# Kernel optimization log

Hardware: AMD Instinct MI355X
Metric: run time of the kernel (lower is better)

## Reference

```python
import jax, jax.numpy as jnp
import numpy as np

B, T, K, H, KS = 8, 2048, 64, 8, 5
PAD = KS - 1  # causal left padding (kernel_size - stride, stride=1)


def setup_inputs() -> dict:
    key = jax.random.key(0)
    ks = jax.random.split(key, 6)
    s = 0.02
    return {
        "x": jax.random.normal(ks[0], (B, T, K), jnp.float32),
        "wq": jax.random.normal(ks[1], (K * H, K, KS), jnp.float32) * s,
        "bq": jnp.zeros((K * H,), jnp.float32),
        "wk": jax.random.normal(ks[2], (K * H, K, KS), jnp.float32) * s,
        "bk": jnp.zeros((K * H,), jnp.float32),
        "wv": jax.random.normal(ks[3], (K * H, K, KS), jnp.float32) * s,
        "wu": jax.random.normal(ks[4], (K, K * H), jnp.float32) * s,
        "bu": jnp.zeros((K,), jnp.float32),
    }


def _causal_conv(x_bkt, w, b=None):
    # x_bkt: [b, k, t]; w: [out_ch, in_ch, ks]; left-pad for causality
    y = jax.lax.conv_general_dilated(
        x_bkt, w, window_strides=(1,), padding=[(PAD, 0)],
        dimension_numbers=("NCH", "OIH", "NCH"))
    if b is not None:
        y = y + b[None, :, None]
    return y


def reference(x, wq, bq, wk, bk, wv, wu, bu):
    b, t, k = x.shape
    xc = jnp.transpose(x, (0, 2, 1))  # [b, k, t]
    # conv output channels k*h are viewed as (k, h): head index varies fastest
    q = _causal_conv(xc, wq, bq).reshape(b, k, H, t)
    kk = _causal_conv(xc, wk, bk).reshape(b, k, H, t)
    v = _causal_conv(xc, wv).reshape(b, k, H, t)
    scale = k ** 0.25
    # scores: [b, h, t_q, t_k]
    w = jnp.einsum("bdht,bdhs->bhts", q / scale, kk / scale)
    mask = jnp.triu(jnp.ones((t, t), bool), 1)  # mask_next=True, mask_diag=False
    w = jnp.where(mask[None, None], -jnp.inf, w)
    w = jax.nn.softmax(w, axis=-1)
    out = jnp.einsum("bhts,bdhs->bthd", w, v)  # [b, t, h, k]
    out = out.reshape(b, t, H * k)  # concat order (h outer, k inner)
    return out @ wu.T + bu
```

## Files before the change

kernel.cpp:

```cpp
#include <hip/hip_runtime.h>
#include <hip/hip_bf16.h>

typedef __attribute__((ext_vector_type(8))) short bf16x8;
typedef __attribute__((ext_vector_type(4))) float f32x4;
typedef __attribute__((ext_vector_type(16))) float f32x16;
typedef __attribute__((ext_vector_type(4))) unsigned int u32x4;
typedef __attribute__((ext_vector_type(2))) unsigned int u32x2;

#define Bn 8
#define Tn 2048
#define Kn 64
#define Hn 8
#define KSn 5
#define CHn 512
#define TPADn 2052

__device__ __forceinline__ unsigned short f2bf(float f) {
    unsigned int x = __builtin_bit_cast(unsigned int, f);
    unsigned int r = (x + 0x7fffu + ((x >> 16) & 1u)) >> 16;
    return (unsigned short)r;
}

__device__ __forceinline__ unsigned int cvt_pk_bf16(float lo, float hi) {
    unsigned int r;
    asm("v_cvt_pk_bf16_f32 %0, %1, %2" : "=v"(r) : "v"(lo), "v"(hi));
    return r;
}

__device__ __forceinline__ float fast_exp2(float x) {
#if __has_builtin(__builtin_amdgcn_exp2f)
    return __builtin_amdgcn_exp2f(x);
#else
    float r;
    asm("v_exp_f32 %0, %1" : "=v"(r) : "v"(x));
    return r;
#endif
}

__device__ __forceinline__ float xhalf_max(float v) {
    return fmaxf(v, __shfl_xor(v, 32));
}
__device__ __forceinline__ float xhalf_add(float v) {
    return v + __shfl_xor(v, 32);
}

__device__ __forceinline__ u32x2 pl32swap(unsigned int x, unsigned int y) {
#if __has_builtin(__builtin_amdgcn_permlane32_swap)
    return __builtin_amdgcn_permlane32_swap(x, y, false, false);
#else
    unsigned int xs = (unsigned int)__shfl_xor((int)x, 32);
    unsigned int ys = (unsigned int)__shfl_xor((int)y, 32);
    int hi = (threadIdx.x & 63) >> 5;
    u32x2 r;
    r[0] = hi ? ys : x;
    r[1] = hi ? y : xs;
    return r;
#endif
}

__device__ __forceinline__ void gload_lds16(const void* g, void* l) {
    __builtin_amdgcn_global_load_lds(
        (const __attribute__((address_space(1))) void*)g,
        (__attribute__((address_space(3))) void*)l, 16, 0, 0);
}

__global__ void prep_kernel(const float* __restrict__ x,
                            const float* __restrict__ wq, const float* __restrict__ bq,
                            const float* __restrict__ wk, const float* __restrict__ bk,
                            const float* __restrict__ wv,
                            const float* __restrict__ wu,
                            unsigned short* __restrict__ x_pad,
                            unsigned short* __restrict__ w2q, unsigned short* __restrict__ w2k,
                            unsigned short* __restrict__ w2v,
                            unsigned short* __restrict__ wu_b,
                            float* __restrict__ bqs, float* __restrict__ bks)
{
    const float inv_scale = 0.424660900144f;
    const int N0 = Bn*TPADn*Kn;
    const int N1 = KSn*CHn*Kn;
    const int total = N0 + 3*N1 + CHn*Kn + 2*CHn;
    for (int i = blockIdx.x*blockDim.x + threadIdx.x; i < total; i += gridDim.x*blockDim.x) {
        if (i < N0) {
            int b = i / (TPADn*Kn);
            int rem = i - b*(TPADn*Kn);
            int p = rem >> 6, ic = rem & 63;
            x_pad[i] = (p < 4) ? (unsigned short)0
                               : f2bf(x[((size_t)b*Tn + (p - 4))*Kn + ic]);
            continue;
        }
        int r = i - N0;
        if (r < 3*N1) {
            int conv = r / N1; int rr = r - conv*N1;
            int j = rr / (CHn*Kn); int rc = rr - j*(CHn*Kn);
            int c = rc >> 6; int ic = rc & 63;
            const float* w = (conv==0) ? wq : ((conv==1) ? wk : wv);
            float s = (conv==2) ? 1.0f : inv_scale;
            unsigned short* dst = (conv==0) ? w2q : ((conv==1) ? w2k : w2v);
            dst[rr] = f2bf(w[(c*Kn + ic)*KSn + j] * s);
            continue;
        }
        r -= 3*N1;
        if (r < CHn*Kn) { wu_b[r] = f2bf(wu[r]); continue; }
        r -= CHn*Kn;
        if (r < CHn) { bqs[r] = bq[r]*inv_scale; continue; }
        r -= CHn;
        bks[r] = bk[r]*inv_scale;
    }
}

__global__ __launch_bounds__(256) void conv_v4(
    const unsigned short* __restrict__ x_pad,
    const unsigned short* __restrict__ w2q, const unsigned short* __restrict__ w2k,
    const unsigned short* __restrict__ w2v,
    const float* __restrict__ bqs, const float* __restrict__ bks,
    unsigned short* __restrict__ q_s, unsigned short* __restrict__ k_s,
    unsigned short* __restrict__ v_t)
{
    __shared__ __align__(16) unsigned short xs[2][72*64];
    __shared__ __align__(16) unsigned short ts[64*64];
    const int tg = blockIdx.x;
    const int c0 = blockIdx.y * 64;
    const int zz = blockIdx.z;
    const int conv = zz >> 3, b = zz & 7;
    const unsigned short* w2 = (conv==0) ? w2q : ((conv==1) ? w2k : w2v);
    const float* bias = (conv==0) ? bqs : ((conv==1) ? bks : nullptr);
    unsigned short* outp = (conv==0) ? q_s : ((conv==1) ? k_s : v_t);
    const int tid = threadIdx.x;
    const int wid = tid >> 6, l = tid & 63;
    const int lr = l & 15, lh = l >> 4;
    const int wt = wid & 1, wc = wid >> 1;

    bf16x8 wf[5][2][2];
    #pragma unroll
    for (int j = 0; j < 5; ++j)
        #pragma unroll
        for (int kk = 0; kk < 2; ++kk)
            #pragma unroll
            for (int n2 = 0; n2 < 2; ++n2)
                wf[j][kk][n2] = *(const bf16x8*)
                    &w2[(j*CHn + c0 + wc*32 + n2*16 + lr)*Kn + kk*32 + lh*8];
    float bv0 = bias ? bias[c0 + wc*32 + lr]      : 0.0f;
    float bv1 = bias ? bias[c0 + wc*32 + 16 + lr] : 0.0f;

    const int swz_row = l >> 3;
    const int src_inrow = ((l & 7) << 4) ^ (swz_row << 4);

    int buf = 0;
    {
        const char* base = (const char*)(x_pad + (size_t)b*TPADn*Kn);
        int p0 = tg*512;
        for (int i = wid; i < 9; i += 4) {
            const char* src = base + (size_t)(p0 + i*8 + swz_row)*128 + src_inrow;
            gload_lds16(src, (char*)&xs[0][0] + i*1024);
        }
    }
    __syncthreads();

    for (int tt = 0; tt < 8; ++tt) {
        const int t0 = (tg*8 + tt)*64;
        if (tt < 7) {
            const char* base = (const char*)(x_pad + (size_t)b*TPADn*Kn);
            int p0 = t0 + 64;
            for (int i = wid; i < 9; i += 4) {
                const char* src = base + (size_t)(p0 + i*8 + swz_row)*128 + src_inrow;
                gload_lds16(src, (char*)&xs[buf^1][0] + i*1024);
            }
        }
        const char* xb = (const char*)&xs[buf][0];
        f32x4 acc[2][2] = {};
        #pragma unroll
        for (int j = 0; j < 5; ++j)
            #pragma unroll
            for (int kk = 0; kk < 2; ++kk) {
                #pragma unroll
                for (int m = 0; m < 2; ++m) {
                    int row = wt*32 + m*16 + lr + j;
                    bf16x8 a = *(const bf16x8*)
                        (xb + row*128 + ((kk*64 + lh*16) ^ ((row & 7) << 4)));
                    acc[m][0] = __builtin_amdgcn_mfma_f32_16x16x32_bf16(a, wf[j][kk][0], acc[m][0], 0, 0, 0);
                    acc[m][1] = __builtin_amdgcn_mfma_f32_16x16x32_bf16(a, wf[j][kk][1], acc[m][1], 0, 0, 0);
                }
            }
        __syncthreads();
        #pragma unroll
        for (int m = 0; m < 2; ++m)
            #pragma unroll
            for (int n2 = 0; n2 < 2; ++n2) {
                float bv = n2 ? bv1 : bv0;
                int cl = wc*32 + n2*16 + lr;
                #pragma unroll
                for (int reg = 0; reg < 4; ++reg) {
                    int tl = wt*32 + m*16 + lh*4 + reg;
                    ts[(tl*64 + cl) ^ ((tl & 7) << 3)] = f2bf(acc[m][n2][reg] + bv);
                }
            }
        __syncthreads();
        if (conv < 2) {
            #pragma unroll
            for (int it = 0; it < 2; ++it) {
                int idx = tid + it*256;
                int tl = idx >> 3, hl = idx & 7;
                unsigned short tmp[8];
                #pragma unroll
                for (int dl = 0; dl < 8; ++dl)
                    tmp[dl] = ts[(tl*64 + hl + 8*dl) ^ ((tl & 7) << 3)];
                size_t el = ((size_t)(b*Hn + hl)*Tn + t0 + tl)*Kn + (c0 >> 3);
                *(u32x4*)&outp[el] = *(u32x4*)tmp;
            }
        } else {
            #pragma unroll
            for (int it = 0; it < 2; ++it) {
                int idx = tid + it*256;
                int tc = idx >> 6, cl2 = idx & 63;
                int hl = cl2 & 7, dl = cl2 >> 3;
                unsigned short tmp[8];
                #pragma unroll
                for (int i2 = 0; i2 < 8; ++i2)
                    tmp[i2] = ts[((tc*8 + i2)*64 + cl2) ^ (((tc*8 + i2) & 7) << 3)];
                size_t el = ((size_t)(b*Hn + hl)*Kn + (c0 >> 3) + dl)*Tn + t0 + tc*8;
                *(u32x4*)&outp[el] = *(u32x4*)tmp;
            }
        }
        buf ^= 1;
    }
}

__global__ __launch_bounds__(256, 4) void attn_kernel(
    const unsigned short* __restrict__ q_s, const unsigned short* __restrict__ k_s,
    const unsigned short* __restrict__ v_t, unsigned short* __restrict__ attn2)
{
    __shared__ __align__(16) unsigned char lds_raw[16384];
    const int tid = threadIdx.x;
    const int wid = tid >> 6, l = tid & 63;
    const int lq = l & 31, hi = l >> 5;
    const int bx = blockIdx.x;
    const int bh = (bx & 7)*8 + ((bx >> 3) & 7);
    const int s4g = (bx >> 6) & 3, g = bx >> 8;
    const int j = (g == 0) ? s4g : (g == 1) ? 15 - s4g : (g == 2) ? 7 - s4g : 8 + s4g;
    const int cmax = 4*j + 3;
    const int cw = 4*j + wid;
    const int qw = cw * 32;
    const unsigned short* qp = q_s + (size_t)bh*Tn*Kn;
    const char* kpc = (const char*)(k_s + (size_t)bh*Tn*Kn);
    const char* vpc = (const char*)(v_t + (size_t)bh*Kn*Tn);
    unsigned short* op = attn2 + (size_t)bh*Tn*Kn;
    const int qg = qw + lq;

    const int krow = wid*8 + (l >> 3);
    const char* kSrc0 = kpc + krow*128 + (((l & 7) ^ (krow & 7)) << 4);
    const char* vSrc0 = vpc + (size_t)krow*8192 + ((l >> 2) & 1)*4096
                      + ((((l & 3) ^ (krow & 3))) << 4);
    const int dstOff = wid*1024;
    auto stage = [&](int pp, int t) {
        gload_lds16(kSrc0 + (size_t)t*4096, lds_raw + pp*4096 + dstOff);
        gload_lds16(vSrc0 + (size_t)t*64,   lds_raw + 8192 + pp*4096 + dstOff);
    };

    bf16x8 qf[4];
    #pragma unroll
    for (int m = 0; m < 4; ++m)
        qf[m] = *(const bf16x8*)&qp[(qw + lq)*Kn + m*16 + hi*8];

    f32x16 o0 = (f32x16)(0.0f), o1 = (f32x16)(0.0f);
    float m_run = -1e30f, l_run = 0.f;

    const int kReadBase = lq*128;
    const int kReadSwz  = (lq & 7) << 4;
    const int vReadBase = (lq >> 1)*128 + (lq & 1)*64;
    const int vSwz = (lq >> 1) & 3;

    stage(0, 0);
    __syncthreads();
    int p = 0;
    for (int t = 0; t <= cmax; ++t) {
        if (t < cmax) stage(p ^ 1, t + 1);
        if (t <= cw) {
            const char* sK = (const char*)lds_raw + p*4096;
            const char* sV = (const char*)lds_raw + 8192 + p*4096;
            bf16x8 kbf[4], vbf[2][2];
            #pragma unroll
            for (int m = 0; m < 4; ++m)
                kbf[m] = *(const bf16x8*)(sK + kReadBase + ((m*32 + hi*16) ^ kReadSwz));
            #pragma unroll
            for (int dn = 0; dn < 2; ++dn)
                #pragma unroll
                for (int ks = 0; ks < 2; ++ks)
                    vbf[dn][ks] = *(const bf16x8*)
                        (sV + dn*2048 + vReadBase + (((ks*2 + hi) ^ vSwz) << 4));
            const int s0 = t*32;
            f32x16 s = (f32x16)(0.0f);
            #pragma unroll
            for (int m = 0; m < 4; ++m)
                s = __builtin_amdgcn_mfma_f32_32x32x16_bf16(kbf[m], qf[m], s, 0, 0, 0);
            if (t == cw) {
                #pragma unroll
                for (int r = 0; r < 16; ++r) {
                    int sg = s0 + (r & 3) + 8*(r >> 2) + 4*hi;
                    if (sg > qg) s[r] = -1e30f;
                }
            }
            float a8[8];
            #pragma unroll
            for (int r = 0; r < 8; ++r) a8[r] = fmaxf(s[r], s[r + 8]);
            float a4_0 = fmaxf(a8[0], a8[4]), a4_1 = fmaxf(a8[1], a8[5]);
            float a4_2 = fmaxf(a8[2], a8[6]), a4_3 = fmaxf(a8[3], a8[7]);
            float mt = fmaxf(fmaxf(a4_0, a4_1), fmaxf(a4_2, a4_3));
            mt = xhalf_max(mt);
            if (!__all(mt <= m_run + 8.0f)) {
                float mn = fmaxf(m_run, mt);
                float alpha = fast_exp2(m_run - mn);
                m_run = mn;
                l_run *= alpha;
                #pragma unroll
                for (int r = 0; r < 16; ++r) { o0[r] *= alpha; o1[r] *= alpha; }
            }
            float ps[4] = {0.f, 0.f, 0.f, 0.f};
            #pragma unroll
            for (int r = 0; r < 16; ++r) {
                float pv = fast_exp2(s[r] - m_run);
                s[r] = pv;
                ps[r & 3] += pv;
            }
            l_run += (ps[0] + ps[1]) + (ps[2] + ps[3]);
            unsigned int W[8];
            #pragma unroll
            for (int rp = 0; rp < 8; ++rp)
                W[rp] = cvt_pk_bf16(s[2*rp], s[2*rp + 1]);
            u32x4 bw[2];
            #pragma unroll
            for (int m = 0; m < 2; ++m)
                #pragma unroll
                for (int jp = 0; jp < 2; ++jp) {
                    u32x2 sw = pl32swap(W[jp + 4*m], W[jp + 4*m + 2]);
                    bw[m][jp]     = sw[0];
                    bw[m][jp + 2] = sw[1];
                }
            o0 = __builtin_amdgcn_mfma_f32_32x32x16_bf16(vbf[0][0], __builtin_bit_cast(bf16x8, bw[0]), o0, 0, 0, 0);
            o0 = __builtin_amdgcn_mfma_f32_32x32x16_bf16(vbf[0][1], __builtin_bit_cast(bf16x8, bw[1]), o0, 0, 0, 0);
            o1 = __builtin_amdgcn_mfma_f32_32x32x16_bf16(vbf[1][0], __builtin_bit_cast(bf16x8, bw[0]), o1, 0, 0, 0);
            o1 = __builtin_amdgcn_mfma_f32_32x32x16_bf16(vbf[1][1], __builtin_bit_cast(bf16x8, bw[1]), o1, 0, 0, 0);
        }
        __syncthreads();
        p ^= 1;
    }

    float l_full = xhalf_add(l_run);
    char* myLds = (char*)lds_raw + wid*4096;
    float inv_l = 1.0f / l_full;
    #pragma unroll
    for (int e = 0; e < 16; e += 2) {
        int dd = (e & 3) + 8*(e >> 2) + 4*hi;
        unsigned int wv0 = cvt_pk_bf16(o0[e]*inv_l, o0[e+1]*inv_l);
        *(unsigned int*)(myLds + ((lq*128 + dd*2)      ^ ((lq & 7) << 4))) = wv0;
        unsigned int wv1 = cvt_pk_bf16(o1[e]*inv_l, o1[e+1]*inv_l);
        *(unsigned int*)(myLds + ((lq*128 + 64 + dd*2) ^ ((lq & 7) << 4))) = wv1;
    }
    int q2 = l >> 1, hf = l & 1;
    #pragma unroll
    for (int o4 = 0; o4 < 4; ++o4) {
        u32x4 vr2 = *(u32x4*)(myLds + ((q2*128 + hf*64 + o4*16) ^ ((q2 & 7) << 4)));
        *(u32x4*)&op[(qw + q2)*Kn + hf*32 + o4*8] = vr2;
    }
}

__global__ __launch_bounds__(256) void proj_kernel(
    const unsigned short* __restrict__ attn, const unsigned short* __restrict__ wu_b,
    const float* __restrict__ bu, float* __restrict__ outp)
{
    __shared__ float red[4*16*66];
    const int r0 = blockIdx.x * 16;
    const int tid = threadIdx.x;
    const int w = tid >> 6, l = tid & 63;
    const int lr = l & 15, lh = l >> 4;
    f32x4 acc[4] = {};
    const int r = r0 + lr;
    const int bb = r >> 11, tt = r & 2047;
    #pragma unroll
    for (int ki = 0; ki < 4; ++ki) {
        int kk = w*4 + ki;
        int ch = kk*32 + lh*8;
        int hh = ch >> 6, dd = ch & 63;
        bf16x8 a = *(const bf16x8*)&attn[(size_t)((bb*Hn + hh)*Tn + tt)*Kn + dd];
        #pragma unroll
        for (int n = 0; n < 4; ++n) {
            bf16x8 bf = *(const bf16x8*)&wu_b[(n*16 + lr)*CHn + ch];
            acc[n] = __builtin_amdgcn_mfma_f32_16x16x32_bf16(a, bf, acc[n], 0, 0, 0);
        }
    }
    #pragma unroll
    for (int n = 0; n < 4; ++n)
        #pragma unroll
        for (int reg = 0; reg < 4; ++reg)
            red[w*1056 + (lh*4 + reg)*66 + n*16 + lr] = acc[n][reg];
    __syncthreads();
    #pragma unroll
    for (int it = 0; it < 4; ++it) {
        int idx = tid + it*256;
        int rl = idx >> 6, ko = idx & 63;
        float s = red[rl*66 + ko] + red[1056 + rl*66 + ko]
                + red[2112 + rl*66 + ko] + red[3168 + rl*66 + ko] + bu[ko];
        outp[(size_t)(r0 + rl)*Kn + ko] = s;
    }
}

extern "C" void kernel_launch(void* const* d_in, const int* in_sizes, int n_in,
                              void* d_out, int out_size, void* d_ws, size_t ws_size,
                              hipStream_t stream)
{
    const float* x  = (const float*)d_in[0];
    const float* wq = (const float*)d_in[1];
    const float* bq = (const float*)d_in[2];
    const float* wk = (const float*)d_in[3];
    const float* bk = (const float*)d_in[4];
    const float* wv = (const float*)d_in[5];
    const float* wu = (const float*)d_in[6];
    const float* bu = (const float*)d_in[7];
    float* outp = (float*)d_out;

    char* ws = (char*)d_ws;
    size_t off = 0;
    auto alloc = [&](size_t bytes) {
        char* p = ws + off;
        off = (off + bytes + 255) & ~(size_t)255;
        return p;
    };
    unsigned short* x_pad = (unsigned short*)alloc((size_t)Bn*TPADn*Kn*2);
    unsigned short* w2q  = (unsigned short*)alloc((size_t)KSn*CHn*Kn*2);
    unsigned short* w2k  = (unsigned short*)alloc((size_t)KSn*CHn*Kn*2);
    unsigned short* w2v  = (unsigned short*)alloc((size_t)KSn*CHn*Kn*2);
    unsigned short* wu_b = (unsigned short*)alloc((size_t)CHn*Kn*2);
    float*  bqs = (float*)alloc(CHn*4);
    float*  bks = (float*)alloc(CHn*4);
    unsigned short* q_s  = (unsigned short*)alloc((size_t)Bn*Hn*Tn*Kn*2);
    unsigned short* k_s  = (unsigned short*)alloc((size_t)Bn*Hn*Tn*Kn*2);
    unsigned short* v_t  = (unsigned short*)alloc((size_t)Bn*Hn*Tn*Kn*2);
    unsigned short* attn = (unsigned short*)alloc((size_t)Bn*Tn*CHn*2);

    prep_kernel<<<2048, 256, 0, stream>>>(x, wq, bq, wk, bk, wv, wu,
                                          x_pad, w2q, w2k, w2v, wu_b, bqs, bks);
    conv_v4<<<dim3(4, 8, 24), 256, 0, stream>>>(
        x_pad, w2q, w2k, w2v, bqs, bks, q_s, k_s, v_t);
    attn_kernel<<<1024, 256, 0, stream>>>(q_s, k_s, v_t, attn);
    proj_kernel<<<(Bn*Tn)/16, 256, 0, stream>>>(attn, wu_b, bu, outp);
}
```

Baseline: 114.8 us.

## Process two 32-key tiles per attention loop iteration with doubled LDS staging

The flash-attention loop now stages and consumes two 32-key K/V tiles per iteration instead of one, doubling the LDS buffer to 32KB. It halves the number of __syncthreads barriers and online-softmax rescale checks per key, and gives the scheduler two independent score MFMA chains to interleave. The cost is more registers and LDS per block, which may lower occupancy under the 4-blocks launch bound. Waves whose diagonal falls on the first tile of a pair also compute a fully masked second tile.

```diff
diff --git a/kernel.cpp b/kernel.cpp
--- a/kernel.cpp
+++ b/kernel.cpp
@@ -229,7 +229,7 @@
     const unsigned short* __restrict__ q_s, const unsigned short* __restrict__ k_s,
     const unsigned short* __restrict__ v_t, unsigned short* __restrict__ attn2)
 {
-    __shared__ __align__(16) unsigned char lds_raw[16384];
+    __shared__ __align__(16) unsigned char lds_raw[32768];
     const int tid = threadIdx.x;
     const int wid = tid >> 6, l = tid & 63;
     const int lq = l & 31, hi = l >> 5;
@@ -237,8 +237,8 @@
     const int bh = (bx & 7)*8 + ((bx >> 3) & 7);
     const int s4g = (bx >> 6) & 3, g = bx >> 8;
     const int j = (g == 0) ? s4g : (g == 1) ? 15 - s4g : (g == 2) ? 7 - s4g : 8 + s4g;
-    const int cmax = 4*j + 3;
     const int cw = 4*j + wid;
+    const int npairs = 2*j + 2;
     const int qw = cw * 32;
     const unsigned short* qp = q_s + (size_t)bh*Tn*Kn;
     const char* kpc = (const char*)(k_s + (size_t)bh*Tn*Kn);
@@ -252,8 +252,10 @@
                       + ((((l & 3) ^ (krow & 3))) << 4);
     const int dstOff = wid*1024;
     auto stage = [&](int pp, int t) {
-        gload_lds16(kSrc0 + (size_t)t*4096, lds_raw + pp*4096 + dstOff);
-        gload_lds16(vSrc0 + (size_t)t*64,   lds_raw + 8192 + pp*4096 + dstOff);
+        gload_lds16(kSrc0 + (size_t)t*4096,       lds_raw + pp*8192 + dstOff);
+        gload_lds16(kSrc0 + (size_t)(t+1)*4096,   lds_raw + pp*8192 + 4096 + dstOff);
+        gload_lds16(vSrc0 + (size_t)t*64,         lds_raw + 16384 + pp*8192 + dstOff);
+        gload_lds16(vSrc0 + (size_t)(t+1)*64,     lds_raw + 16384 + pp*8192 + 4096 + dstOff);
     };
 
     bf16x8 qf[4];
@@ -272,36 +274,59 @@
     stage(0, 0);
     __syncthreads();
     int p = 0;
-    for (int t = 0; t <= cmax; ++t) {
-        if (t < cmax) stage(p ^ 1, t + 1);
+    for (int pi = 0; pi < npairs; ++pi) {
+        const int t = 2*pi;
+        if (pi + 1 < npairs) stage(p ^ 1, t + 2);
         if (t <= cw) {
-            const char* sK = (const char*)lds_raw + p*4096;
-            const char* sV = (const char*)lds_raw + 8192 + p*4096;
-            bf16x8 kbf[4], vbf[2][2];
+            const char* sK0 = (const char*)lds_raw + p*8192;
+            const char* sK1 = sK0 + 4096;
+            const char* sV0 = (const char*)lds_raw + 16384 + p*8192;
+            const char* sV1 = sV0 + 4096;
+            bf16x8 k0[4], k1[4], v0[2][2], v1[2][2];
+            #pragma unroll
+            for (int m = 0; m < 4; ++m) {
+                k0[m] = *(const bf16x8*)(sK0 + kReadBase + ((m*32 + hi*16) ^ kReadSwz));
+                k1[m] = *(const bf16x8*)(sK1 + kReadBase + ((m*32 + hi*16) ^ kReadSwz));
+            }
+            #pragma unroll
+            for (int dn = 0; dn < 2; ++dn)
+                #pragma unroll
+                for (int ks = 0; ks < 2; ++ks) {
+                    v0[dn][ks] = *(const bf16x8*)
+                        (sV0 + dn*2048 + vReadBase + (((ks*2 + hi) ^ vSwz) << 4));
+                    v1[dn][ks] = *(const bf16x8*)
+                        (sV1 + dn*2048 + vReadBase + (((ks*2 + hi) ^ vSwz) << 4));
+                }
+            f32x16 s = (f32x16)(0.0f), s2 = (f32x16)(0.0f);
             #pragma unroll
             for (int m = 0; m < 4; ++m)
-                kbf[m] = *(const bf16x8*)(sK + kReadBase + ((m*32 + hi*16) ^ kReadSwz));
-            #pragma unroll
-            for (int dn = 0; dn < 2; ++dn)
-                #pragma unroll
-                for (int ks = 0; ks < 2; ++ks)
-                    vbf[dn][ks] = *(const bf16x8*)
-                        (sV + dn*2048 + vReadBase + (((ks*2 + hi) ^ vSwz) << 4));
-            const int s0 = t*32;
-            f32x16 s = (f32x16)(0.0f);
+                s  = __builtin_amdgcn_mfma_f32_32x32x16_bf16(k0[m], qf[m], s, 0, 0, 0);
             #pragma unroll
             for (int m = 0; m < 4; ++m)
-                s = __builtin_amdgcn_mfma_f32_32x32x16_bf16(kbf[m], qf[m], s, 0, 0, 0);
+                s2 = __builtin_amdgcn_mfma_f32_32x32x16_bf16(k1[m], qf[m], s2, 0, 0, 0);
             if (t == cw) {
+                const int s0g = t*32;
                 #pragma unroll
                 for (int r = 0; r < 16; ++r) {
-                    int sg = s0 + (r & 3) + 8*(r >> 2) + 4*hi;
+                    int sg = s0g + (r & 3) + 8*(r >> 2) + 4*hi;
                     if (sg > qg) s[r] = -1e30f;
                 }
             }
+            if (t + 1 > cw) {
+                #pragma unroll
+                for (int r = 0; r < 16; ++r) s2[r] = -1e30f;
+            } else if (t + 1 == cw) {
+                const int s0g = (t + 1)*32;
+                #pragma unroll
+                for (int r = 0; r < 16; ++r) {
+                    int sg = s0g + (r & 3) + 8*(r >> 2) + 4*hi;
+                    if (sg > qg) s2[r] = -1e30f;
+                }
+            }
             float a8[8];
             #pragma unroll
-            for (int r = 0; r < 8; ++r) a8[r] = fmaxf(s[r], s[r + 8]);
+            for (int r = 0; r < 8; ++r)
+                a8[r] = fmaxf(fmaxf(s[r], s[r + 8]), fmaxf(s2[r], s2[r + 8]));
             float a4_0 = fmaxf(a8[0], a8[4]), a4_1 = fmaxf(a8[1], a8[5]);
             float a4_2 = fmaxf(a8[2], a8[6]), a4_3 = fmaxf(a8[3], a8[7]);
             float mt = fmaxf(fmaxf(a4_0, a4_1), fmaxf(a4_2, a4_3));
@@ -318,15 +343,18 @@
             #pragma unroll
             for (int r = 0; r < 16; ++r) {
                 float pv = fast_exp2(s[r] - m_run);
-                s[r] = pv;
-                ps[r & 3] += pv;
+                s[r] = pv; ps[r & 3] += pv;
+                float pv2 = fast_exp2(s2[r] - m_run);
+                s2[r] = pv2; ps[r & 3] += pv2;
             }
             l_run += (ps[0] + ps[1]) + (ps[2] + ps[3]);
-            unsigned int W[8];
-            #pragma unroll
-            for (int rp = 0; rp < 8; ++rp)
-                W[rp] = cvt_pk_bf16(s[2*rp], s[2*rp + 1]);
-            u32x4 bw[2];
+            unsigned int W[8], W2[8];
+            #pragma unroll
+            for (int rp = 0; rp < 8; ++rp) {
+                W[rp]  = cvt_pk_bf16(s[2*rp],  s[2*rp + 1]);
+                W2[rp] = cvt_pk_bf16(s2[2*rp], s2[2*rp + 1]);
+            }
+            u32x4 bw[2], bw2[2];
             #pragma unroll
             for (int m = 0; m < 2; ++m)
                 #pragma unroll
@@ -334,11 +362,18 @@
                     u32x2 sw = pl32swap(W[jp + 4*m], W[jp + 4*m + 2]);
                     bw[m][jp]     = sw[0];
                     bw[m][jp + 2] = sw[1];
-                }
-            o0 = __builtin_amdgcn_mfma_f32_32x32x16_bf16(vbf[0][0], __builtin_bit_cast(bf16x8, bw[0]), o0, 0, 0, 0);
-            o0 = __builtin_amdgcn_mfma_f32_32x32x16_bf16(vbf[0][1], __builtin_bit_cast(bf16x8, bw[1]), o0, 0, 0, 0);
-            o1 = __builtin_amdgcn_mfma_f32_32x32x16_bf16(vbf[1][0], __builtin_bit_cast(bf16x8, bw[0]), o1, 0, 0, 0);
-            o1 = __builtin_amdgcn_mfma_f32_32x32x16_bf16(vbf[1][1], __builtin_bit_cast(bf16x8, bw[1]), o1, 0, 0, 0);
+                    u32x2 sw2 = pl32swap(W2[jp + 4*m], W2[jp + 4*m + 2]);
+                    bw2[m][jp]     = sw2[0];
+                    bw2[m][jp + 2] = sw2[1];
+                }
+            o0 = __builtin_amdgcn_mfma_f32_32x32x16_bf16(v0[0][0], __builtin_bit_cast(bf16x8, bw[0]),  o0, 0, 0, 0);
+            o0 = __builtin_amdgcn_mfma_f32_32x32x16_bf16(v0[0][1], __builtin_bit_cast(bf16x8, bw[1]),  o0, 0, 0, 0);
+            o0 = __builtin_amdgcn_mfma_f32_32x32x16_bf16(v1[0][0], __builtin_bit_cast(bf16x8, bw2[0]), o0, 0, 0, 0);
+            o0 = __builtin_amdgcn_mfma_f32_32x32x16_bf16(v1[0][1], __builtin_bit_cast(bf16x8, bw2[1]), o0, 0, 0, 0);
+            o1 = __builtin_amdgcn_mfma_f32_32x32x16_bf16(v0[1][0], __builtin_bit_cast(bf16x8, bw[0]),  o1, 0, 0, 0);
+            o1 = __builtin_amdgcn_mfma_f32_32x32x16_bf16(v0[1][1], __builtin_bit_cast(bf16x8, bw[1]),  o1, 0, 0, 0);
+            o1 = __builtin_amdgcn_mfma_f32_32x32x16_bf16(v1[1][0], __builtin_bit_cast(bf16x8, bw2[0]), o1, 0, 0, 0);
+            o1 = __builtin_amdgcn_mfma_f32_32x32x16_bf16(v1[1][1], __builtin_bit_cast(bf16x8, bw2[1]), o1, 0, 0, 0);
         }
         __syncthreads();
         p ^= 1;
```

Measured after the change: 137.3 us, median of 2. 19.7% more time.
